# Kernel tuning notes

Measured on AMD Instinct MI355X. Metric: run time of the kernel, lower is better.

Reference implementation:

```python
import jax, jax.numpy as jnp
import numpy as np

HIDDEN = 1024
N_HEADS = 16
HEAD_DIM = 64
LOCAL_WINDOW = 1024
GLOBAL_STRIDE = 512


def _sparse_mask(seq_len):
    # local sliding window (half-window each side), strided global columns, causal
    i = jnp.arange(seq_len)[:, None]
    j = jnp.arange(seq_len)[None, :]
    diff = i - j
    local = jnp.abs(diff) <= (LOCAL_WINDOW // 2)
    glob = (j % GLOBAL_STRIDE) == 0
    causal = diff >= 0
    return (local | glob) & causal  # [S, S] bool


def setup_inputs() -> dict:
    key = jax.random.key(0)
    k0, k1, k2, k3, k4 = jax.random.split(key, 5)
    B, S = 1, 2048
    scale = 1.0 / np.sqrt(HIDDEN)
    return {
        "hidden_states": jax.random.normal(k0, (B, S, HIDDEN), dtype=jnp.float32),
        "w_q": jax.random.normal(k1, (HIDDEN, N_HEADS * HEAD_DIM), dtype=jnp.float32) * scale,
        "w_k": jax.random.normal(k2, (HIDDEN, N_HEADS * HEAD_DIM), dtype=jnp.float32) * scale,
        "w_v": jax.random.normal(k3, (HIDDEN, N_HEADS * HEAD_DIM), dtype=jnp.float32) * scale,
        "w_o": jax.random.normal(k4, (N_HEADS * HEAD_DIM, HIDDEN), dtype=jnp.float32) * scale,
    }


def reference(hidden_states, w_q, w_k, w_v, w_o):
    B, S, _ = hidden_states.shape

    def shape(x):  # [B,S,H*D] -> [B,H,S,D]
        return x.reshape(B, S, N_HEADS, HEAD_DIM).transpose(0, 2, 1, 3)

    q = shape(hidden_states @ w_q)
    k = shape(hidden_states @ w_k)
    v = shape(hidden_states @ w_v)

    scores = jnp.einsum("bhqd,bhkd->bhqk", q, k) / np.sqrt(HEAD_DIM)
    mask = _sparse_mask(S)  # [S,S]
    scores = jnp.where(mask[None, None], scores, -jnp.inf)
    attn = jax.nn.softmax(scores, axis=-1)
    out = jnp.einsum("bhqk,bhkd->bhqd", attn, v)
    out = out.transpose(0, 2, 1, 3).reshape(B, S, N_HEADS * HEAD_DIM)
    return out @ w_o
```

## Files before the change

kernel.cpp:

```cpp
#include <hip/hip_runtime.h>
#include <hip/hip_bf16.h>

#define SEQ 2048
#define HID 1024
#define NH 16
#define HD 64
#define QKVLD 3072

typedef __attribute__((ext_vector_type(8))) short bf16x8;
typedef __attribute__((ext_vector_type(4))) float f32x4;

__device__ __forceinline__ unsigned short f2bf(float f) {
  unsigned int x = __float_as_uint(f);
  x += 0x7fffu + ((x >> 16) & 1u);
  return (unsigned short)(x >> 16);
}

__device__ __forceinline__ unsigned int pkbf(float a, float b) {
  union { __hip_bfloat162 h2; unsigned int u; } cvt;
  cvt.h2 = __float22bfloat162_rn(make_float2(a, b));
  return cvt.u;
}

__device__ __forceinline__ void gld_lds16(const void* g, void* l) {
  __builtin_amdgcn_global_load_lds((__attribute__((address_space(1))) void*)g,
                                   (__attribute__((address_space(3))) void*)l, 16, 0, 0);
}

__global__ void prep(const float* __restrict__ X, const float* __restrict__ Wq,
                     const float* __restrict__ Wk, const float* __restrict__ Wv,
                     const float* __restrict__ Wo, unsigned short* __restrict__ Xb,
                     unsigned short* __restrict__ WtQKV, unsigned short* __restrict__ WtO) {
  const int z = blockIdx.z;
  if (z == 4) {
    int bid = blockIdx.y * 32 + blockIdx.x;
    int t = threadIdx.y * 32 + threadIdx.x;
    size_t base = (size_t)bid * 2048 + t * 4;
#pragma unroll
    for (int half = 0; half < 2; half++) {
      float4 v = *(const float4*)(X + base + half * 1024);
      *(uint2*)(Xb + base + half * 1024) = make_uint2(pkbf(v.x, v.y), pkbf(v.z, v.w));
    }
    return;
  }
  __shared__ float tile[32][33];
  const float* S = (z == 0) ? Wq : (z == 1) ? Wk : (z == 2) ? Wv : Wo;
  unsigned short* D = (z < 3) ? (WtQKV + (size_t)z * HID * HID) : WtO;
  const float scale = (z == 0) ? 0.125f : 1.0f;
  int r0 = blockIdx.y * 32, c0 = blockIdx.x * 32;
  int tx = threadIdx.x, ty = threadIdx.y;
#pragma unroll
  for (int k = 0; k < 4; k++)
    tile[ty + k * 8][tx] = S[(size_t)(r0 + ty + k * 8) * HID + c0 + tx];
  __syncthreads();
#pragma unroll
  for (int k = 0; k < 4; k++)
    D[(size_t)(c0 + ty + k * 8) * HID + r0 + tx] = f2bf(scale * tile[tx][ty + k * 8]);
}

template <int MI, int BN, int BK, int GX, int RW, int XB, int WPE, int OUT>
__global__ __launch_bounds__(256, WPE) void gemm_bt(const unsigned short* __restrict__ A,
                                                    const unsigned short* __restrict__ Bt,
                                                    void* __restrict__ Cout,
                                                    unsigned short* __restrict__ Vout,
                                                    int M, int N, int K) {
  constexpr int NI = BN / 32;
  constexpr int TM = MI * 32;
  constexpr int KC = BK / 8;
  static_assert(KC == 8, "8-chunk XOR swizzle requires BK=64");
  __shared__ unsigned short As[2][TM * BK];
  __shared__ unsigned short Bs[2][BN * BK];
  const int tid = threadIdx.x;
  const int lane = tid & 63;
  const int w = tid >> 6;
  const int wm = w >> 1, wn = w & 1;
  const int quad = lane >> 4, l16 = lane & 15;

  const int lin = blockIdx.x + GX * blockIdx.y;
  const int xcd = lin & 7, idx = lin >> 3;
  const int bx = (xcd & 3) * RW + (idx % RW);
  const int by = (xcd >> 2) * (XB / RW) + (idx / RW);
  const int bm = by * TM, bn = bx * BN;

  f32x4 acc[MI][NI] = {};

  auto stage = [&](int k0, int b) {
#pragma unroll
    for (int c = tid; c < TM * KC; c += 256) {
      int r = c / KC, kc = c % KC;
      int g = kc ^ (r & 7);
      gld_lds16(A + (size_t)(bm + r) * K + k0 + g * 8, &As[b][c * 8]);
    }
#pragma unroll
    for (int c = tid; c < BN * KC; c += 256) {
      int r = c / KC, kc = c % KC;
      int g = kc ^ (r & 7);
      gld_lds16(Bt + (size_t)(bn + r) * K + k0 + g * 8, &Bs[b][c * 8]);
    }
  };

  const int NT = K / BK;
  stage(0, 0);
  __syncthreads();

  for (int t = 0; t < NT; ++t) {
    if (t + 1 < NT) stage((t + 1) * BK, (t + 1) & 1);
    const unsigned short* AsB = &As[t & 1][0];
    const unsigned short* BsB = &Bs[t & 1][0];
#pragma unroll
    for (int ks = 0; ks < BK / 32; ks++) {
      bf16x8 af[MI], bfr[NI];
#pragma unroll
      for (int mi = 0; mi < MI; mi++) {
        int m = wm * (MI * 16) + mi * 16 + l16;
        af[mi] = *(const bf16x8*)(AsB + (m * KC + ((ks * 4 + quad) ^ (m & 7))) * 8);
      }
#pragma unroll
      for (int ni = 0; ni < NI; ni++) {
        int n = wn * (BN / 2) + ni * 16 + l16;
        bfr[ni] = *(const bf16x8*)(BsB + (n * KC + ((ks * 4 + quad) ^ (n & 7))) * 8);
      }
#pragma unroll
      for (int mi = 0; mi < MI; mi++)
#pragma unroll
        for (int ni = 0; ni < NI; ni++)
          acc[mi][ni] = __builtin_amdgcn_mfma_f32_16x16x32_bf16(af[mi], bfr[ni], acc[mi][ni], 0, 0, 0);
    }
    __syncthreads();
  }

#pragma unroll
  for (int mi = 0; mi < MI; mi++) {
#pragma unroll
    for (int ni = 0; ni < NI; ni++) {
      int row = bm + wm * (MI * 16) + mi * 16 + quad * 4;
      int col = bn + wn * (BN / 2) + ni * 16 + l16;
      if (OUT == 0) {
#pragma unroll
        for (int r = 0; r < 4; r++)
          ((float*)Cout)[(size_t)(row + r) * N + col] = acc[mi][ni][r];
      } else {
        if (col < 2 * HID) {
#pragma unroll
          for (int r = 0; r < 4; r++)
            ((unsigned short*)Cout)[(size_t)(row + r) * N + col] = f2bf(acc[mi][ni][r]);
        } else {
          *(uint2*)(Vout + (size_t)(col - 2 * HID) * SEQ + row) =
              make_uint2(pkbf(acc[mi][ni][0], acc[mi][ni][1]),
                         pkbf(acc[mi][ni][2], acc[mi][ni][3]));
        }
      }
    }
  }
}

__global__ __launch_bounds__(256, 3) void attn_sparse(const unsigned short* __restrict__ QKV,
                                                      const unsigned short* __restrict__ VtG,
                                                      unsigned short* __restrict__ AttO) {
  __shared__ unsigned short Ks[2][64 * 64];
  __shared__ unsigned short Vt[2][64 * 64];
  __shared__ unsigned short Pw[4][16 * 72];
  const int lin = blockIdx.x + 32 * blockIdx.y;
  const int xcd = lin & 7, slot = lin >> 3;
  const int h = slot >> 2;
  const int qbase = (xcd * 4 + (slot & 3)) * 64;
  const int tid = threadIdx.x;
  const int lane = tid & 63, w = tid >> 6;
  const int quad = lane >> 4, l16 = lane & 15;
  const int qrow0 = qbase + w * 16;
  unsigned short* pws = &Pw[w][0];

  bf16x8 aq[2];
  {
    const unsigned short* qp = QKV + (size_t)(qrow0 + l16) * QKVLD + h * HD + quad * 8;
    aq[0] = *(const bf16x8*)qp;
    aq[1] = *(const bf16x8*)(qp + 32);
  }

  f32x4 accO[4] = {};
  float lsum = 0.f;

  const int jlo = (qbase >= 512) ? (qbase - 512) : 0;
  const int ng = (jlo > 0) ? ((jlo + 511) >> 9) : 0;
  const int ntl = ((qbase - jlo) >> 6) + 1;

  auto stage = [&](int j0, int b) {
#pragma unroll
    for (int c = tid; c < 512; c += 256) {
      int r = c >> 3, kc = c & 7;
      int g = kc ^ (r & 7);
      gld_lds16(QKV + (size_t)(j0 + r) * QKVLD + HID + h * HD + g * 8, &Ks[b][c * 8]);
      gld_lds16(VtG + (size_t)(h * HD + r) * SEQ + j0 + g * 8, &Vt[b][c * 8]);
    }
  };

  stage(jlo, 0);
  __syncthreads();

  for (int t = 0; t < ntl; t++) {
    if (t + 1 < ntl) stage(jlo + (t + 1) * 64, (t + 1) & 1);
    const unsigned short* KsB = Ks[t & 1];
    const unsigned short* VtB = Vt[t & 1];
    const int j0 = jlo + t * 64;

    f32x4 s[4] = {};
#pragma unroll
    for (int nj = 0; nj < 4; nj++) {
      int row = nj * 16 + l16;
#pragma unroll
      for (int ks = 0; ks < 2; ks++) {
        bf16x8 ak = *(const bf16x8*)(KsB + (row * 8 + ((ks * 4 + quad) ^ (row & 7))) * 8);
        s[nj] = __builtin_amdgcn_mfma_f32_16x16x32_bf16(ak, aq[ks], s[nj], 0, 0, 0);
      }
    }

    const bool isdiag = (t == ntl - 1);
    const bool istrail = (t == 0) && (qbase >= 512);
    const int trailg = (istrail && ((j0 & 511) == 0)) ? 1 : 0;
    const int db = qrow0 + l16 - j0 - quad * 4;
#pragma unroll
    for (int nj = 0; nj < 4; nj++) {
      float p[4];
#pragma unroll
      for (int r = 0; r < 4; r++) {
        float x = s[nj][r];
        int d = db - nj * 16 - r;
        bool valid = true;
        if (isdiag) valid = (d >= 0);
        else if (istrail) valid = (d <= 512) || (trailg && (nj * 16 + quad * 4 + r) == 0);
        x = valid ? x : -1e30f;
        p[r] = __expf(x);
        lsum += p[r];
      }
      *(uint2*)(pws + l16 * 72 + nj * 16 + quad * 4) =
          make_uint2(pkbf(p[0], p[1]), pkbf(p[2], p[3]));
    }

#pragma unroll
    for (int kk = 0; kk < 2; kk++) {
      bf16x8 bp = *(const bf16x8*)(pws + l16 * 72 + kk * 32 + quad * 8);
#pragma unroll
      for (int nd = 0; nd < 4; nd++) {
        int row = nd * 16 + l16;
        bf16x8 av = *(const bf16x8*)(VtB + (row * 8 + ((kk * 4 + quad) ^ (row & 7))) * 8);
        accO[nd] = __builtin_amdgcn_mfma_f32_16x16x32_bf16(av, bp, accO[nd], 0, 0, 0);
      }
    }
    __syncthreads();
  }

  if (ng > 0) {
    if (tid < ng * 8) {
      int r = tid >> 3, kc = tid & 7;
      int g = kc ^ (r & 7);
      *(uint4*)(&Ks[0][tid * 8]) =
          *(const uint4*)(QKV + ((size_t)r << 9) * QKVLD + HID + h * HD + g * 8);
    }
    if (tid < ng * 64) {
      int d = tid & 63, c = tid >> 6;
      Vt[0][(d * 8 + (d & 7)) * 8 + c] = VtG[(size_t)(h * HD + d) * SEQ + ((size_t)c << 9)];
    }
    __syncthreads();
    f32x4 s0 = {};
#pragma unroll
    for (int ks = 0; ks < 2; ks++) {
      bf16x8 ak = *(const bf16x8*)(&Ks[0][(l16 * 8 + ((ks * 4 + quad) ^ (l16 & 7))) * 8]);
      s0 = __builtin_amdgcn_mfma_f32_16x16x32_bf16(ak, aq[ks], s0, 0, 0, 0);
    }
    float p[4];
#pragma unroll
    for (int r = 0; r < 4; r++) {
      p[r] = ((quad * 4 + r) < ng) ? __expf(s0[r]) : 0.f;
      lsum += p[r];
    }
    *(uint2*)(pws + l16 * 72 + quad * 4) = make_uint2(pkbf(p[0], p[1]), pkbf(p[2], p[3]));
    *(uint2*)(pws + l16 * 72 + 16 + quad * 4) = make_uint2(0, 0);
    bf16x8 bp = *(const bf16x8*)(pws + l16 * 72 + quad * 8);
#pragma unroll
    for (int nd = 0; nd < 4; nd++) {
      int row = nd * 16 + l16;
      bf16x8 av = *(const bf16x8*)(&Vt[0][(row * 8 + (quad ^ (row & 7))) * 8]);
      accO[nd] = __builtin_amdgcn_mfma_f32_16x16x32_bf16(av, bp, accO[nd], 0, 0, 0);
    }
  }

  lsum += __shfl_xor(lsum, 16);
  lsum += __shfl_xor(lsum, 32);
  const float rl = 1.0f / lsum;
  const int i = qrow0 + l16;
#pragma unroll
  for (int nd = 0; nd < 4; nd++) {
    *(uint2*)(AttO + (size_t)i * HID + h * HD + nd * 16 + quad * 4) =
        make_uint2(pkbf(accO[nd][0] * rl, accO[nd][1] * rl),
                   pkbf(accO[nd][2] * rl, accO[nd][3] * rl));
  }
}

extern "C" void kernel_launch(void* const* d_in, const int* in_sizes, int n_in,
                              void* d_out, int out_size, void* d_ws, size_t ws_size,
                              hipStream_t stream) {
  const float* X  = (const float*)d_in[0];
  const float* Wq = (const float*)d_in[1];
  const float* Wk = (const float*)d_in[2];
  const float* Wv = (const float*)d_in[3];
  const float* Wo = (const float*)d_in[4];
  float* out = (float*)d_out;

  unsigned short* Xb    = (unsigned short*)d_ws;
  unsigned short* WtQKV = Xb + (size_t)SEQ * HID;
  unsigned short* WtO   = WtQKV + (size_t)QKVLD * HID;
  unsigned short* QKV   = WtO + (size_t)HID * HID;
  unsigned short* VtG   = QKV + (size_t)SEQ * QKVLD;
  unsigned short* AttO  = VtG + (size_t)HID * SEQ;

  prep<<<dim3(32, 32, 5), dim3(32, 8), 0, stream>>>(X, Wq, Wk, Wv, Wo, Xb, WtQKV, WtO);

  gemm_bt<4, 96, 64, 32, 8, 64, 2, 2><<<dim3(32, 16), dim3(256), 0, stream>>>(
      Xb, WtQKV, QKV, VtG, SEQ, QKVLD, HID);

  attn_sparse<<<dim3(SEQ / 64, NH), dim3(256), 0, stream>>>(QKV, VtG, AttO);

  gemm_bt<2, 64, 64, 16, 4, 64, 2, 0><<<dim3(16, 32), dim3(256), 0, stream>>>(
      AttO, WtO, out, nullptr, SEQ, HID, HID);
}
```

Measured before the change: 123.3 us.

## Fuse all four stages into one cooperative persistent kernel with grid syncs

The prep, QKV GEMM, sparse attention and output GEMM kernels become one cooperative kernel of 512 blocks, with grid.sync() between stages. Each stage reuses a single shared-memory buffer and the same block index remapping. The prep stage is re-tiled so each block does a fixed share of the conversion and transpose work. This removes three kernel launch boundaries and their gaps. In exchange it adds grid-wide barriers, fixes occupancy at two blocks per CU with a 56KB static LDS buffer, and depends on cooperative launch residency.

Result: slower. 312.3 us (+153.3%).

```diff
diff --git a/kernel.cpp b/kernel.cpp
--- a/kernel.cpp
+++ b/kernel.cpp
@@ -1,5 +1,8 @@
 #include <hip/hip_runtime.h>
 #include <hip/hip_bf16.h>
+#include <hip/hip_cooperative_groups.h>
+
+namespace cg = cooperative_groups;
 
 #define SEQ 2048
 #define HID 1024
@@ -27,56 +30,57 @@
                                    (__attribute__((address_space(3))) void*)l, 16, 0, 0);
 }
 
-__global__ void prep(const float* __restrict__ X, const float* __restrict__ Wq,
-                     const float* __restrict__ Wk, const float* __restrict__ Wv,
-                     const float* __restrict__ Wo, unsigned short* __restrict__ Xb,
-                     unsigned short* __restrict__ WtQKV, unsigned short* __restrict__ WtO) {
-  const int z = blockIdx.z;
-  if (z == 4) {
-    int bid = blockIdx.y * 32 + blockIdx.x;
-    int t = threadIdx.y * 32 + threadIdx.x;
-    size_t base = (size_t)bid * 2048 + t * 4;
-#pragma unroll
-    for (int half = 0; half < 2; half++) {
-      float4 v = *(const float4*)(X + base + half * 1024);
-      *(uint2*)(Xb + base + half * 1024) = make_uint2(pkbf(v.x, v.y), pkbf(v.z, v.w));
-    }
-    return;
-  }
-  __shared__ float tile[32][33];
-  const float* S = (z == 0) ? Wq : (z == 1) ? Wk : (z == 2) ? Wv : Wo;
-  unsigned short* D = (z < 3) ? (WtQKV + (size_t)z * HID * HID) : WtO;
-  const float scale = (z == 0) ? 0.125f : 1.0f;
-  int r0 = blockIdx.y * 32, c0 = blockIdx.x * 32;
-  int tx = threadIdx.x, ty = threadIdx.y;
-#pragma unroll
-  for (int k = 0; k < 4; k++)
-    tile[ty + k * 8][tx] = S[(size_t)(r0 + ty + k * 8) * HID + c0 + tx];
-  __syncthreads();
-#pragma unroll
-  for (int k = 0; k < 4; k++)
-    D[(size_t)(c0 + ty + k * 8) * HID + r0 + tx] = f2bf(scale * tile[tx][ty + k * 8]);
-}
-
-template <int MI, int BN, int BK, int GX, int RW, int XB, int WPE, int OUT>
-__global__ __launch_bounds__(256, WPE) void gemm_bt(const unsigned short* __restrict__ A,
-                                                    const unsigned short* __restrict__ Bt,
-                                                    void* __restrict__ Cout,
-                                                    unsigned short* __restrict__ Vout,
-                                                    int M, int N, int K) {
+
+__device__ void prep_body(int bid, int tid, char* smem, const float* X, const float* Wq,
+                          const float* Wk, const float* Wv, const float* Wo,
+                          unsigned short* Xb, unsigned short* WtQKV, unsigned short* WtO) {
+  {
+    size_t base0 = (size_t)(bid * 2) * 2048 + (size_t)tid * 4;
+#pragma unroll
+    for (int u = 0; u < 2; u++) {
+#pragma unroll
+      for (int half = 0; half < 2; half++) {
+        size_t base = base0 + u * 2048 + half * 1024;
+        float4 v = *(const float4*)(X + base);
+        *(uint2*)(Xb + base) = make_uint2(pkbf(v.x, v.y), pkbf(v.z, v.w));
+      }
+    }
+  }
+  float(*tile)[33] = (float(*)[33])smem;
+  const int tx = tid & 31, ty = tid >> 5;
+  for (int i = 0; i < 8; i++) {
+    int wt = bid * 8 + i;
+    int z = wt >> 10, t = wt & 1023;
+    const float* S = (z == 0) ? Wq : (z == 1) ? Wk : (z == 2) ? Wv : Wo;
+    unsigned short* D = (z < 3) ? (WtQKV + (size_t)z * HID * HID) : WtO;
+    const float scale = (z == 0) ? 0.125f : 1.0f;
+    int r0 = (t >> 5) * 32, c0 = (t & 31) * 32;
+    __syncthreads();
+#pragma unroll
+    for (int k = 0; k < 4; k++)
+      tile[ty + k * 8][tx] = S[(size_t)(r0 + ty + k * 8) * HID + c0 + tx];
+    __syncthreads();
+#pragma unroll
+    for (int k = 0; k < 4; k++)
+      D[(size_t)(c0 + ty + k * 8) * HID + r0 + tx] = f2bf(scale * tile[tx][ty + k * 8]);
+  }
+}
+
+template <int MI, int BN, int BK, int RW, int XB, int OUT>
+__device__ void gemm_body(int lin, int tid, char* smem, const unsigned short* A,
+                          const unsigned short* Bt, void* Cout, unsigned short* Vout,
+                          int M, int N, int K) {
   constexpr int NI = BN / 32;
   constexpr int TM = MI * 32;
   constexpr int KC = BK / 8;
   static_assert(KC == 8, "8-chunk XOR swizzle requires BK=64");
-  __shared__ unsigned short As[2][TM * BK];
-  __shared__ unsigned short Bs[2][BN * BK];
-  const int tid = threadIdx.x;
+  unsigned short* As = (unsigned short*)smem;
+  unsigned short* Bs = As + 2 * TM * BK;
   const int lane = tid & 63;
   const int w = tid >> 6;
   const int wm = w >> 1, wn = w & 1;
   const int quad = lane >> 4, l16 = lane & 15;
 
-  const int lin = blockIdx.x + GX * blockIdx.y;
   const int xcd = lin & 7, idx = lin >> 3;
   const int bx = (xcd & 3) * RW + (idx % RW);
   const int by = (xcd >> 2) * (XB / RW) + (idx / RW);
@@ -89,13 +93,13 @@
     for (int c = tid; c < TM * KC; c += 256) {
       int r = c / KC, kc = c % KC;
       int g = kc ^ (r & 7);
-      gld_lds16(A + (size_t)(bm + r) * K + k0 + g * 8, &As[b][c * 8]);
+      gld_lds16(A + (size_t)(bm + r) * K + k0 + g * 8, As + b * TM * BK + c * 8);
     }
 #pragma unroll
     for (int c = tid; c < BN * KC; c += 256) {
       int r = c / KC, kc = c % KC;
       int g = kc ^ (r & 7);
-      gld_lds16(Bt + (size_t)(bn + r) * K + k0 + g * 8, &Bs[b][c * 8]);
+      gld_lds16(Bt + (size_t)(bn + r) * K + k0 + g * 8, Bs + b * BN * BK + c * 8);
     }
   };
 
@@ -105,8 +109,8 @@
 
   for (int t = 0; t < NT; ++t) {
     if (t + 1 < NT) stage((t + 1) * BK, (t + 1) & 1);
-    const unsigned short* AsB = &As[t & 1][0];
-    const unsigned short* BsB = &Bs[t & 1][0];
+    const unsigned short* AsB = As + (t & 1) * TM * BK;
+    const unsigned short* BsB = Bs + (t & 1) * BN * BK;
 #pragma unroll
     for (int ks = 0; ks < BK / 32; ks++) {
       bf16x8 af[MI], bfr[NI];
@@ -154,21 +158,18 @@
   }
 }
 
-__global__ __launch_bounds__(256, 3) void attn_sparse(const unsigned short* __restrict__ QKV,
-                                                      const unsigned short* __restrict__ VtG,
-                                                      unsigned short* __restrict__ AttO) {
-  __shared__ unsigned short Ks[2][64 * 64];
-  __shared__ unsigned short Vt[2][64 * 64];
-  __shared__ unsigned short Pw[4][16 * 72];
-  const int lin = blockIdx.x + 32 * blockIdx.y;
+__device__ void attn_body(int lin, int tid, char* smem, const unsigned short* QKV,
+                          const unsigned short* VtG, unsigned short* AttO) {
+  unsigned short* Ks = (unsigned short*)smem;
+  unsigned short* Vt = Ks + 2 * 64 * 64;
+  unsigned short* Pw = Vt + 2 * 64 * 64;
   const int xcd = lin & 7, slot = lin >> 3;
   const int h = slot >> 2;
   const int qbase = (xcd * 4 + (slot & 3)) * 64;
-  const int tid = threadIdx.x;
   const int lane = tid & 63, w = tid >> 6;
   const int quad = lane >> 4, l16 = lane & 15;
   const int qrow0 = qbase + w * 16;
-  unsigned short* pws = &Pw[w][0];
+  unsigned short* pws = Pw + w * 16 * 72;
 
   bf16x8 aq[2];
   {
@@ -189,8 +190,8 @@
     for (int c = tid; c < 512; c += 256) {
       int r = c >> 3, kc = c & 7;
       int g = kc ^ (r & 7);
-      gld_lds16(QKV + (size_t)(j0 + r) * QKVLD + HID + h * HD + g * 8, &Ks[b][c * 8]);
-      gld_lds16(VtG + (size_t)(h * HD + r) * SEQ + j0 + g * 8, &Vt[b][c * 8]);
+      gld_lds16(QKV + (size_t)(j0 + r) * QKVLD + HID + h * HD + g * 8, Ks + b * 4096 + c * 8);
+      gld_lds16(VtG + (size_t)(h * HD + r) * SEQ + j0 + g * 8, Vt + b * 4096 + c * 8);
     }
   };
 
@@ -199,8 +200,8 @@
 
   for (int t = 0; t < ntl; t++) {
     if (t + 1 < ntl) stage(jlo + (t + 1) * 64, (t + 1) & 1);
-    const unsigned short* KsB = Ks[t & 1];
-    const unsigned short* VtB = Vt[t & 1];
+    const unsigned short* KsB = Ks + (t & 1) * 4096;
+    const unsigned short* VtB = Vt + (t & 1) * 4096;
     const int j0 = jlo + t * 64;
 
     f32x4 s[4] = {};
@@ -253,18 +254,18 @@
     if (tid < ng * 8) {
       int r = tid >> 3, kc = tid & 7;
       int g = kc ^ (r & 7);
-      *(uint4*)(&Ks[0][tid * 8]) =
+      *(uint4*)(Ks + tid * 8) =
           *(const uint4*)(QKV + ((size_t)r << 9) * QKVLD + HID + h * HD + g * 8);
     }
     if (tid < ng * 64) {
       int d = tid & 63, c = tid >> 6;
-      Vt[0][(d * 8 + (d & 7)) * 8 + c] = VtG[(size_t)(h * HD + d) * SEQ + ((size_t)c << 9)];
+      Vt[(d * 8 + (d & 7)) * 8 + c] = VtG[(size_t)(h * HD + d) * SEQ + ((size_t)c << 9)];
     }
     __syncthreads();
     f32x4 s0 = {};
 #pragma unroll
     for (int ks = 0; ks < 2; ks++) {
-      bf16x8 ak = *(const bf16x8*)(&Ks[0][(l16 * 8 + ((ks * 4 + quad) ^ (l16 & 7))) * 8]);
+      bf16x8 ak = *(const bf16x8*)(Ks + (l16 * 8 + ((ks * 4 + quad) ^ (l16 & 7))) * 8);
       s0 = __builtin_amdgcn_mfma_f32_16x16x32_bf16(ak, aq[ks], s0, 0, 0, 0);
     }
     float p[4];
@@ -279,7 +280,7 @@
 #pragma unroll
     for (int nd = 0; nd < 4; nd++) {
       int row = nd * 16 + l16;
-      bf16x8 av = *(const bf16x8*)(&Vt[0][(row * 8 + (quad ^ (row & 7))) * 8]);
+      bf16x8 av = *(const bf16x8*)(Vt + (row * 8 + (quad ^ (row & 7))) * 8);
       accO[nd] = __builtin_amdgcn_mfma_f32_16x16x32_bf16(av, bp, accO[nd], 0, 0, 0);
     }
   }
@@ -294,6 +295,32 @@
         make_uint2(pkbf(accO[nd][0] * rl, accO[nd][1] * rl),
                    pkbf(accO[nd][2] * rl, accO[nd][3] * rl));
   }
+}
+
+__global__ __launch_bounds__(256, 2) void fused(const float* __restrict__ X,
+                                                const float* __restrict__ Wq,
+                                                const float* __restrict__ Wk,
+                                                const float* __restrict__ Wv,
+                                                const float* __restrict__ Wo,
+                                                float* __restrict__ out,
+                                                unsigned short* __restrict__ Xb,
+                                                unsigned short* __restrict__ WtQKV,
+                                                unsigned short* __restrict__ WtO,
+                                                unsigned short* __restrict__ QKV,
+                                                unsigned short* __restrict__ VtG,
+                                                unsigned short* __restrict__ AttO) {
+  __shared__ alignas(16) char smem[57344];
+  cg::grid_group grid = cg::this_grid();
+  const int bid = blockIdx.x;
+  const int tid = threadIdx.x;
+
+  prep_body(bid, tid, smem, X, Wq, Wk, Wv, Wo, Xb, WtQKV, WtO);
+  grid.sync();
+  gemm_body<4, 96, 64, 8, 64, 2>(bid, tid, smem, Xb, WtQKV, QKV, VtG, SEQ, QKVLD, HID);
+  grid.sync();
+  attn_body(bid, tid, smem, QKV, VtG, AttO);
+  grid.sync();
+  gemm_body<2, 64, 64, 4, 64, 0>(bid, tid, smem, AttO, WtO, out, nullptr, SEQ, HID, HID);
 }
 
 extern "C" void kernel_launch(void* const* d_in, const int* in_sizes, int n_in,
@@ -313,13 +340,8 @@
   unsigned short* VtG   = QKV + (size_t)SEQ * QKVLD;
   unsigned short* AttO  = VtG + (size_t)HID * SEQ;
 
-  prep<<<dim3(32, 32, 5), dim3(32, 8), 0, stream>>>(X, Wq, Wk, Wv, Wo, Xb, WtQKV, WtO);
-
-  gemm_bt<4, 96, 64, 32, 8, 64, 2, 2><<<dim3(32, 16), dim3(256), 0, stream>>>(
-      Xb, WtQKV, QKV, VtG, SEQ, QKVLD, HID);
-
-  attn_sparse<<<dim3(SEQ / 64, NH), dim3(256), 0, stream>>>(QKV, VtG, AttO);
-
-  gemm_bt<2, 64, 64, 16, 4, 64, 2, 0><<<dim3(16, 32), dim3(256), 0, stream>>>(
-      AttO, WtO, out, nullptr, SEQ, HID, HID);
-}
+  void* args[] = {(void*)&X, (void*)&Wq, (void*)&Wk, (void*)&Wv, (void*)&Wo, (void*)&out,
+                  (void*)&Xb, (void*)&WtQKV, (void*)&WtO, (void*)&QKV, (void*)&VtG,
+                  (void*)&AttO};
+  hipLaunchCooperativeKernel((const void*)fused, dim3(512), dim3(256), args, 0, stream);
+}
```
